# Performance work log

Measured on AMD Instinct MI355X. Metric: run time of the kernel, lower is better.

## Reference

```python
import jax, jax.numpy as jnp
import numpy as np


def setup_inputs() -> dict:
    key = jax.random.key(0)
    ks = jax.random.split(key, 6)
    B, R, H, E, D = 64, 2048, 1024, 512, 1024
    hidden_states = jax.random.normal(ks[0], (B, H), dtype=jnp.float32)
    att_feats = jax.random.normal(ks[1], (B, R, D), dtype=jnp.float32)
    p_att_feats = jax.random.normal(ks[2], (B, R, E), dtype=jnp.float32)
    att_masks = jnp.zeros((B, R), dtype=jnp.float32)  # additive mask; zeros = unmasked
    w_h = jax.random.normal(ks[3], (H, E), dtype=jnp.float32) * (1.0 / np.sqrt(H))
    w_alpha = jax.random.normal(ks[4], (E,), dtype=jnp.float32) * (1.0 / np.sqrt(E))
    return {"hidden_states": hidden_states, "att_feats": att_feats,
            "p_att_feats": p_att_feats, "att_masks": att_masks,
            "w_h": w_h, "w_alpha": w_alpha}


def reference(hidden_states, att_feats, p_att_feats, att_masks, w_h, w_alpha):
    # w_h(hidden_states): [B, E], broadcast over regions R
    wh = hidden_states @ w_h                      # [B, E]
    alpha = jnp.tanh(wh[:, None, :] + p_att_feats)  # [B, R, E]
    # w_alpha reduces E -> scalar per region
    alpha = jnp.einsum('bre,e->br', alpha, w_alpha)  # [B, R]
    alpha = alpha + att_masks                     # additive mask
    alpha = jax.nn.softmax(alpha, axis=-1)        # [B, R]
    # weighted sum over regions: bmm(alpha[:,None,:], att_feats).squeeze(1)
    att = jnp.einsum('br,brd->bd', alpha, att_feats)  # [B, D]
    return att
```

## Files before the change

### kernel.cpp

```cpp
#include <hip/hip_runtime.h>
#include <math.h>

#define BB 64
#define RR 2048
#define HH 1024
#define EE 512
#define DD 1024
#define RCH 32
#define RPC (RR / RCH)
#define NRW 4

typedef float f32x4 __attribute__((ext_vector_type(4)));

__device__ __forceinline__ float fast_tanh(float x) {
    float e = __expf(2.0f * x);
    return 1.0f - 2.0f * __builtin_amdgcn_rcpf(e + 1.0f);
}

__global__ __launch_bounds__(128) void k_wh(const float* __restrict__ hidden,
                                            const float* __restrict__ w_h,
                                            float* __restrict__ wh) {
    __shared__ float sh[HH];
    const int b = blockIdx.x;
    const int e = blockIdx.y * 128 + threadIdx.x;
    for (int h = threadIdx.x; h < HH; h += 128) sh[h] = hidden[b * HH + h];
    __syncthreads();
    float acc = 0.f;
#pragma unroll 8
    for (int h = 0; h < HH; ++h) acc = fmaf(sh[h], w_h[h * EE + e], acc);
    wh[b * EE + e] = acc;
}

__global__ __launch_bounds__(256) void k_logits(const float* __restrict__ p_att,
                                                const float* __restrict__ wh,
                                                const float* __restrict__ w_alpha,
                                                const float* __restrict__ mask,
                                                float* __restrict__ logits) {
    const int wave = threadIdx.x >> 6;
    const int lane = threadIdx.x & 63;
    const long long row0 = ((long long)blockIdx.x * 4 + wave) * NRW;
    const int b = (int)(row0 >> 11);
    const float* __restrict__ whb = wh + b * EE;
    const f32x4 wh0 = *(const f32x4*)(whb + lane * 4);
    const f32x4 wh1 = *(const f32x4*)(whb + 256 + lane * 4);
    const f32x4 wa0 = *(const f32x4*)(w_alpha + lane * 4);
    const f32x4 wa1 = *(const f32x4*)(w_alpha + 256 + lane * 4);
    const f32x4* __restrict__ pbase = (const f32x4*)(p_att + row0 * EE);
#pragma unroll
    for (int r = 0; r < NRW; ++r) {
        const f32x4* __restrict__ pr = pbase + (long long)r * (EE / 4);
        f32x4 p0 = __builtin_nontemporal_load(pr + lane);
        f32x4 p1 = __builtin_nontemporal_load(pr + 64 + lane);
        float s;
        s = fast_tanh(p0.x + wh0.x) * wa0.x;
        s = fmaf(fast_tanh(p0.y + wh0.y), wa0.y, s);
        s = fmaf(fast_tanh(p0.z + wh0.z), wa0.z, s);
        s = fmaf(fast_tanh(p0.w + wh0.w), wa0.w, s);
        s = fmaf(fast_tanh(p1.x + wh1.x), wa1.x, s);
        s = fmaf(fast_tanh(p1.y + wh1.y), wa1.y, s);
        s = fmaf(fast_tanh(p1.z + wh1.z), wa1.z, s);
        s = fmaf(fast_tanh(p1.w + wh1.w), wa1.w, s);
#pragma unroll
        for (int off = 32; off; off >>= 1) s += __shfl_xor(s, off);
        if (lane == 0) {
            const long long row = row0 + r;
            logits[row] = s + mask[row];
        }
    }
}

__global__ __launch_bounds__(256) void k_softmax(const float* __restrict__ logits,
                                                 float* __restrict__ alpha) {
    const int b = blockIdx.x;
    const int t = threadIdx.x;
    const int wave = t >> 6, lane = t & 63;
    __shared__ float smax[4], ssum[4];
    float v[8];
    float m = -INFINITY;
#pragma unroll
    for (int i = 0; i < 8; ++i) {
        v[i] = logits[b * RR + i * 256 + t];
        m = fmaxf(m, v[i]);
    }
#pragma unroll
    for (int off = 32; off; off >>= 1) m = fmaxf(m, __shfl_xor(m, off));
    if (lane == 0) smax[wave] = m;
    __syncthreads();
    m = fmaxf(fmaxf(smax[0], smax[1]), fmaxf(smax[2], smax[3]));
    float s = 0.f;
#pragma unroll
    for (int i = 0; i < 8; ++i) {
        v[i] = __expf(v[i] - m);
        s += v[i];
    }
#pragma unroll
    for (int off = 32; off; off >>= 1) s += __shfl_xor(s, off);
    if (lane == 0) ssum[wave] = s;
    __syncthreads();
    s = ssum[0] + ssum[1] + ssum[2] + ssum[3];
    const float inv = 1.0f / s;
#pragma unroll
    for (int i = 0; i < 8; ++i) alpha[b * RR + i * 256 + t] = v[i] * inv;
}

__global__ __launch_bounds__(256) void k_att_partial(const float* __restrict__ alpha,
                                                     const float* __restrict__ feats,
                                                     float* __restrict__ part) {
    const int b = blockIdx.x;
    const int rc = blockIdx.y;
    const int t = threadIdx.x;
    __shared__ float sa[RPC];
    if (t < RPC) sa[t] = alpha[b * RR + rc * RPC + t];
    __syncthreads();
    const f32x4* __restrict__ fp =
        (const f32x4*)(feats + ((long long)b * RR + (long long)rc * RPC) * DD) + t;
    f32x4 acc = {0.f, 0.f, 0.f, 0.f};
#pragma unroll 8
    for (int r = 0; r < RPC; ++r) {
        const float a = sa[r];
        f32x4 f = __builtin_nontemporal_load(fp + r * (DD / 4));
        acc.x = fmaf(a, f.x, acc.x);
        acc.y = fmaf(a, f.y, acc.y);
        acc.z = fmaf(a, f.z, acc.z);
        acc.w = fmaf(a, f.w, acc.w);
    }
    *((f32x4*)(part + (long long)(b * RCH + rc) * DD) + t) = acc;
}

__global__ __launch_bounds__(256) void k_att_reduce(const float* __restrict__ part,
                                                    float* __restrict__ out) {
    const int idx = blockIdx.x * 256 + threadIdx.x;
    const int b = idx >> 10;
    const int d = idx & 1023;
    float s = 0.f;
#pragma unroll
    for (int rc = 0; rc < RCH; ++rc) s += part[(long long)(b * RCH + rc) * DD + d];
    out[idx] = s;
}

extern "C" void kernel_launch(void* const* d_in, const int* in_sizes, int n_in,
                              void* d_out, int out_size, void* d_ws, size_t ws_size,
                              hipStream_t stream) {
    const float* hidden  = (const float*)d_in[0];
    const float* feats   = (const float*)d_in[1];
    const float* p_att   = (const float*)d_in[2];
    const float* mask    = (const float*)d_in[3];
    const float* w_h     = (const float*)d_in[4];
    const float* w_alpha = (const float*)d_in[5];
    float* out = (float*)d_out;

    char* ws = (char*)d_ws;
    float* wh     = (float*)(ws);
    float* logits = (float*)(ws + (size_t)131072);
    float* alpha  = (float*)(ws + (size_t)655360);
    float* part   = (float*)(ws + (size_t)1179648);

    k_wh<<<dim3(BB, 4), 128, 0, stream>>>(hidden, w_h, wh);
    k_logits<<<(BB * RR) / (4 * NRW), 256, 0, stream>>>(p_att, wh, w_alpha, mask, logits);
    k_softmax<<<BB, 256, 0, stream>>>(logits, alpha);
    k_att_partial<<<dim3(BB, RCH), 256, 0, stream>>>(alpha, feats, part);
    k_att_reduce<<<(BB * DD) / 256, 256, 0, stream>>>(part, out);
}
```

Measured before the change: 191.3 us.

## Fuse logits, softmax and weighted sum into one kernel with deferred normalization

Computes exp of the masked logits per region chunk inside the same block that accumulates the weighted feature sum. The block writes unnormalized numerators and per-chunk denominators, and a final kernel sums and divides them. This removes the separate softmax and logits/alpha passes and their launches. It drops max subtraction, which risks overflow for large logits. k_wh is also split across four waves reducing over the hidden dimension.

```diff
diff --git a/kernel.cpp b/kernel.cpp
--- a/kernel.cpp
+++ b/kernel.cpp
@@ -6,9 +6,9 @@
 #define HH 1024
 #define EE 512
 #define DD 1024
-#define RCH 32
-#define RPC (RR / RCH)
-#define NRW 4
+#define RC 32
+#define RPB (RR / RC)
+#define RPW (RPB / 4)
 
 typedef float f32x4 __attribute__((ext_vector_type(4)));
 
@@ -17,40 +17,51 @@
     return 1.0f - 2.0f * __builtin_amdgcn_rcpf(e + 1.0f);
 }
 
-__global__ __launch_bounds__(128) void k_wh(const float* __restrict__ hidden,
+__global__ __launch_bounds__(256) void k_wh(const float* __restrict__ hidden,
                                             const float* __restrict__ w_h,
                                             float* __restrict__ wh) {
     __shared__ float sh[HH];
+    __shared__ float sred[4][64];
     const int b = blockIdx.x;
-    const int e = blockIdx.y * 128 + threadIdx.x;
-    for (int h = threadIdx.x; h < HH; h += 128) sh[h] = hidden[b * HH + h];
+    const int t = threadIdx.x;
+    const int lane = t & 63, hseg = t >> 6;
+    const int e = blockIdx.y * 64 + lane;
+    for (int h = t; h < HH; h += 256) sh[h] = hidden[b * HH + h];
     __syncthreads();
+    const int h0 = hseg * 256;
     float acc = 0.f;
 #pragma unroll 8
-    for (int h = 0; h < HH; ++h) acc = fmaf(sh[h], w_h[h * EE + e], acc);
-    wh[b * EE + e] = acc;
+    for (int h = 0; h < 256; ++h) acc = fmaf(sh[h0 + h], w_h[(h0 + h) * EE + e], acc);
+    sred[hseg][lane] = acc;
+    __syncthreads();
+    if (t < 64)
+        wh[b * EE + blockIdx.y * 64 + t] =
+            (sred[0][t] + sred[1][t]) + (sred[2][t] + sred[3][t]);
 }
 
-__global__ __launch_bounds__(256) void k_logits(const float* __restrict__ p_att,
-                                                const float* __restrict__ wh,
-                                                const float* __restrict__ w_alpha,
-                                                const float* __restrict__ mask,
-                                                float* __restrict__ logits) {
-    const int wave = threadIdx.x >> 6;
-    const int lane = threadIdx.x & 63;
-    const long long row0 = ((long long)blockIdx.x * 4 + wave) * NRW;
-    const int b = (int)(row0 >> 11);
+__global__ __launch_bounds__(256) void k_fused(const float* __restrict__ p_att,
+                                               const float* __restrict__ feats,
+                                               const float* __restrict__ wh,
+                                               const float* __restrict__ w_alpha,
+                                               const float* __restrict__ mask,
+                                               float* __restrict__ num,
+                                               float* __restrict__ den) {
+    __shared__ float sw[RPB];
+    const int b = blockIdx.x, rc = blockIdx.y;
+    const int t = threadIdx.x, wave = t >> 6, lane = t & 63;
+    const int r0 = rc * RPB;
+
     const float* __restrict__ whb = wh + b * EE;
     const f32x4 wh0 = *(const f32x4*)(whb + lane * 4);
     const f32x4 wh1 = *(const f32x4*)(whb + 256 + lane * 4);
     const f32x4 wa0 = *(const f32x4*)(w_alpha + lane * 4);
     const f32x4 wa1 = *(const f32x4*)(w_alpha + 256 + lane * 4);
-    const f32x4* __restrict__ pbase = (const f32x4*)(p_att + row0 * EE);
-#pragma unroll
-    for (int r = 0; r < NRW; ++r) {
-        const f32x4* __restrict__ pr = pbase + (long long)r * (EE / 4);
-        f32x4 p0 = __builtin_nontemporal_load(pr + lane);
-        f32x4 p1 = __builtin_nontemporal_load(pr + 64 + lane);
+    const long long rowb = (long long)b * RR + r0 + wave * RPW;
+    const f32x4* __restrict__ pb = (const f32x4*)(p_att + rowb * EE);
+#pragma unroll 4
+    for (int rr = 0; rr < RPW; ++rr) {
+        f32x4 p0 = __builtin_nontemporal_load(pb + rr * (EE / 4) + lane);
+        f32x4 p1 = __builtin_nontemporal_load(pb + rr * (EE / 4) + 64 + lane);
         float s;
         s = fast_tanh(p0.x + wh0.x) * wa0.x;
         s = fmaf(fast_tanh(p0.y + wh0.y), wa0.y, s);
@@ -62,80 +73,45 @@
         s = fmaf(fast_tanh(p1.w + wh1.w), wa1.w, s);
 #pragma unroll
         for (int off = 32; off; off >>= 1) s += __shfl_xor(s, off);
-        if (lane == 0) {
-            const long long row = row0 + r;
-            logits[row] = s + mask[row];
-        }
+        if (lane == 0) sw[wave * RPW + rr] = __expf(s + mask[rowb + rr]);
     }
-}
+    __syncthreads();
 
-__global__ __launch_bounds__(256) void k_softmax(const float* __restrict__ logits,
-                                                 float* __restrict__ alpha) {
-    const int b = blockIdx.x;
-    const int t = threadIdx.x;
-    const int wave = t >> 6, lane = t & 63;
-    __shared__ float smax[4], ssum[4];
-    float v[8];
-    float m = -INFINITY;
-#pragma unroll
-    for (int i = 0; i < 8; ++i) {
-        v[i] = logits[b * RR + i * 256 + t];
-        m = fmaxf(m, v[i]);
-    }
-#pragma unroll
-    for (int off = 32; off; off >>= 1) m = fmaxf(m, __shfl_xor(m, off));
-    if (lane == 0) smax[wave] = m;
-    __syncthreads();
-    m = fmaxf(fmaxf(smax[0], smax[1]), fmaxf(smax[2], smax[3]));
-    float s = 0.f;
-#pragma unroll
-    for (int i = 0; i < 8; ++i) {
-        v[i] = __expf(v[i] - m);
-        s += v[i];
-    }
-#pragma unroll
-    for (int off = 32; off; off >>= 1) s += __shfl_xor(s, off);
-    if (lane == 0) ssum[wave] = s;
-    __syncthreads();
-    s = ssum[0] + ssum[1] + ssum[2] + ssum[3];
-    const float inv = 1.0f / s;
-#pragma unroll
-    for (int i = 0; i < 8; ++i) alpha[b * RR + i * 256 + t] = v[i] * inv;
-}
-
-__global__ __launch_bounds__(256) void k_att_partial(const float* __restrict__ alpha,
-                                                     const float* __restrict__ feats,
-                                                     float* __restrict__ part) {
-    const int b = blockIdx.x;
-    const int rc = blockIdx.y;
-    const int t = threadIdx.x;
-    __shared__ float sa[RPC];
-    if (t < RPC) sa[t] = alpha[b * RR + rc * RPC + t];
-    __syncthreads();
-    const f32x4* __restrict__ fp =
-        (const f32x4*)(feats + ((long long)b * RR + (long long)rc * RPC) * DD) + t;
+    const f32x4* __restrict__ fb =
+        (const f32x4*)(feats + ((long long)b * RR + r0) * DD) + t;
     f32x4 acc = {0.f, 0.f, 0.f, 0.f};
 #pragma unroll 8
-    for (int r = 0; r < RPC; ++r) {
-        const float a = sa[r];
-        f32x4 f = __builtin_nontemporal_load(fp + r * (DD / 4));
+    for (int r = 0; r < RPB; ++r) {
+        const float a = sw[r];
+        f32x4 f = __builtin_nontemporal_load(fb + r * (DD / 4));
         acc.x = fmaf(a, f.x, acc.x);
         acc.y = fmaf(a, f.y, acc.y);
         acc.z = fmaf(a, f.z, acc.z);
         acc.w = fmaf(a, f.w, acc.w);
     }
-    *((f32x4*)(part + (long long)(b * RCH + rc) * DD) + t) = acc;
+    ((f32x4*)(num + (long long)(b * RC + rc) * DD))[t] = acc;
+    if (t == 0) {
+        float d = 0.f;
+#pragma unroll
+        for (int r = 0; r < RPB; ++r) d += sw[r];
+        den[b * RC + rc] = d;
+    }
 }
 
-__global__ __launch_bounds__(256) void k_att_reduce(const float* __restrict__ part,
-                                                    float* __restrict__ out) {
+__global__ __launch_bounds__(256) void k_out(const float* __restrict__ num,
+                                             const float* __restrict__ den,
+                                             float* __restrict__ out) {
     const int idx = blockIdx.x * 256 + threadIdx.x;
     const int b = idx >> 10;
     const int d = idx & 1023;
-    float s = 0.f;
+    float ds = 0.f;
 #pragma unroll
-    for (int rc = 0; rc < RCH; ++rc) s += part[(long long)(b * RCH + rc) * DD + d];
-    out[idx] = s;
+    for (int rc = 0; rc < RC; ++rc) ds += den[b * RC + rc];
+    float ns = 0.f;
+#pragma unroll
+    for (int rc = 0; rc < RC; ++rc)
+        ns += num[((long long)(b * RC + rc) << 10) + d];
+    out[idx] = ns / ds;
 }
 
 extern "C" void kernel_launch(void* const* d_in, const int* in_sizes, int n_in,
@@ -150,14 +126,11 @@
     float* out = (float*)d_out;
 
     char* ws = (char*)d_ws;
-    float* wh     = (float*)(ws);
-    float* logits = (float*)(ws + (size_t)131072);
-    float* alpha  = (float*)(ws + (size_t)655360);
-    float* part   = (float*)(ws + (size_t)1179648);
+    float* wh  = (float*)(ws);
+    float* num = (float*)(ws + (size_t)131072);
+    float* den = (float*)(ws + (size_t)(131072 + 8388608));
 
-    k_wh<<<dim3(BB, 4), 128, 0, stream>>>(hidden, w_h, wh);
-    k_logits<<<(BB * RR) / (4 * NRW), 256, 0, stream>>>(p_att, wh, w_alpha, mask, logits);
-    k_softmax<<<BB, 256, 0, stream>>>(logits, alpha);
-    k_att_partial<<<dim3(BB, RCH), 256, 0, stream>>>(alpha, feats, part);
-    k_att_reduce<<<(BB * DD) / 256, 256, 0, stream>>>(part, out);
+    k_wh<<<dim3(BB, EE / 64), 256, 0, stream>>>(hidden, w_h, wh);
+    k_fused<<<dim3(BB, RC), 256, 0, stream>>>(p_att, feats, wh, w_alpha, mask, num, den);
+    k_out<<<(BB * DD) / 256, 256, 0, stream>>>(num, den, out);
 }
```

Result: faster. 162.1 us (-15.2%).
